# Performance work log

Hardware: AMD Instinct MI355X
Metric: run time of the kernel (lower is better)

Reference implementation:

```python
import jax, jax.numpy as jnp
import numpy as np

# Static dims (match init_kwargs)
N = 20000      # ngene_in == ngene_out
H = 4          # nheads
DIN = 32       # nhidatt_in
D = 32         # nhidatt
E = 640000     # edges per graph
NMETA = 64
SLOPE = 0.2    # DGL GATConv default negative_slope

# hypernetwork_in flat output split sizes (a, w, b, a_out, w_out, b_out)
# a: H*1*(2*DIN)*1=256, w: H*1*DIN=128, b: H*DIN=128, a_out: 1*(2*DIN)=64,
# w_out: (DIN*H)*DIN=4096, b_out: 1*DIN=32  -> total 4704
HIN_OFF = np.cumsum([0, 256, 128, 128, 64, 4096, 32])
# hypernetwork_out1 (L=2 att layers): a: H*3*(2*D)=768, w: H*(DIN+2*D)*D=12288,
# b: H*3*D=384, a_out: 3*(2*D)=192, w_out: (3*D*H)*D=12288, b_out: 3*D=96 -> 26016
HOUT_OFF = np.cumsum([0, 768, 12288, 384, 192, 12288, 96])


def gatconv(src, dst, x, fc_w, bias, attn_l, attn_r, heads, dout):
    """DGL-style GATConv on an edge list (src -> dst), sum-aggregation at dst."""
    feat = (x @ fc_w.T).reshape(N, heads, dout)          # [N,H,D]
    el = jnp.sum(feat * attn_l, axis=-1)                 # [N,H]
    er = jnp.sum(feat * attn_r, axis=-1)                 # [N,H]
    e = jax.nn.leaky_relu(el[src] + er[dst], SLOPE)      # [E,H]
    m = jax.ops.segment_max(e, dst, num_segments=N)      # edge-softmax (stable)
    m = jnp.where(jnp.isfinite(m), m, 0.0)
    ex = jnp.exp(e - m[dst])
    s = jax.ops.segment_sum(ex, dst, num_segments=N)
    alpha = ex / (s[dst] + 1e-9)                         # [E,H]
    out = jax.ops.segment_sum(alpha[:, :, None] * feat[src], dst, num_segments=N)
    return out + bias.reshape(1, heads, dout)            # [N,H,D]


def _split(h, offs):
    return [h[offs[i]:offs[i + 1]] for i in range(len(offs) - 1)]


def setup_inputs() -> dict:
    key = jax.random.key(0)
    ks = jax.random.split(key, 12)
    return {
        "X_in1": jax.random.normal(ks[0], (N,), jnp.float32),
        "metadata_in1": jax.random.normal(ks[1], (NMETA,), jnp.float32),
        "metadata_trg": jax.random.normal(ks[2], (NMETA,), jnp.float32),
        "W_hin": jax.random.normal(ks[3], (NMETA, 4704), jnp.float32) * 0.05,
        "b_hin": jax.random.normal(ks[4], (4704,), jnp.float32) * 0.05,
        "W_hout": jax.random.normal(ks[5], (NMETA, 26016), jnp.float32) * 0.05,
        "b_hout": jax.random.normal(ks[6], (26016,), jnp.float32) * 0.05,
        "src_in": jax.random.randint(ks[7], (E,), 0, N, jnp.int32),
        "dst_in": jax.random.randint(ks[8], (E,), 0, N, jnp.int32),
        "src_trg": jax.random.randint(ks[9], (E,), 0, N, jnp.int32),
        "dst_trg": jax.random.randint(ks[10], (E,), 0, N, jnp.int32),
    }


def reference(X_in1, metadata_in1, metadata_trg, W_hin, b_hin, W_hout, b_hout,
              src_in, dst_in, src_trg, dst_trg):
    # ---- hypernetwork_in(metadata_in1): generate input-GAT params ----
    h = metadata_in1 @ W_hin + b_hin
    a_f, w_f, b_f, ao_f, wo_f, bo_f = _split(h, HIN_OFF)
    a_in = a_f.reshape(H, 1, 2 * DIN, 1)
    w_in = w_f.reshape(H, 1, DIN)
    b_in = b_f.reshape(H, DIN)
    a_out_in = ao_f.reshape(1, 2 * DIN)
    w_out_in = wo_f.reshape(DIN * H, DIN)
    b_out_in = bo_f.reshape(1, DIN)

    # ---- gat() helper on g_in1 (attentions1 + out_att1) ----
    a_tmp = a_in[:, 0, :, :].reshape(2, H, -1)           # exact torch reshape
    w_tmp = w_in[:, :1, :].reshape(-1, 1)                # [H*DIN, 1]
    b_tmp = b_in[:, :DIN].reshape(-1)                    # [H*DIN]
    ao_tmp = a_out_in[0, :].reshape(2, -1)
    wo_tmp = w_out_in[:DIN * H, :].reshape(-1, DIN * H)  # [DIN, DIN*H]
    bo_tmp = b_out_in[0, :]

    x = X_in1[:N].reshape(-1, 1)
    z = gatconv(src_in, dst_in, x, w_tmp, b_tmp,
                a_tmp[0].reshape(1, H, -1), a_tmp[1].reshape(1, H, -1),
                H, DIN).reshape(N, -1)                   # [N, H*DIN]
    z_1 = jax.nn.elu(gatconv(src_in, dst_in, z, wo_tmp, bo_tmp,
                             ao_tmp[0].reshape(1, 1, -1), ao_tmp[1].reshape(1, 1, -1),
                             1, DIN)).reshape(N, -1)     # [N, DIN]

    # ---- hypernetwork_out1(metadata_trg): params for attentions3/4 ----
    h2 = metadata_trg @ W_hout + b_hout
    a_f, w_f, b_f, ao_f, wo_f, bo_f = _split(h2, HOUT_OFF)
    a = a_f.reshape(H, -1, 2 * D, 1)                     # [H, 3, 2D, 1]
    w = w_f.reshape(H, -1, D)                            # [H, DIN+2D, D]
    b = b_f.reshape(H, -1)                               # [H, 3D]
    a_out = ao_f.reshape(-1, 2 * D)                      # [3, 2D]
    w_out = wo_f.reshape(-1, D)                          # [3*D*H, D]
    b_out = bo_f.reshape(-1, D)                          # [3, D]

    # ---- attentions3 / out_att3 on g_trg_in ----
    a_t = a[:, 0, :, :].reshape(2, H, -1)
    w_t = w[:, :DIN, :].reshape(-1, DIN)                 # [H*D, DIN]
    b_t = b[:, :D].reshape(-1)
    ao_t = a_out[0, :].reshape(2, -1)
    wo_t = w_out[:D * H, :].reshape(-1, D * H)
    bo_t = b_out[0, :]
    z2 = gatconv(src_trg, dst_trg, z_1, w_t, b_t,
                 a_t[0].reshape(1, H, -1), a_t[1].reshape(1, H, -1),
                 H, D).reshape(N, -1)
    z2 = jax.nn.elu(gatconv(src_trg, dst_trg, z2, wo_t, bo_t,
                            ao_t[0].reshape(1, 1, -1), ao_t[1].reshape(1, 1, -1),
                            1, D)).reshape(N, D)

    # ---- attentions4 / out_att4 on g_trg_in ----
    a_t2 = a[:, 1, :, :].reshape(2, H, -1)
    w_t2 = w[:, DIN:DIN + D, :].reshape(-1, D)
    b_t2 = b[:, D:2 * D].reshape(-1)
    ao_t2 = a_out[1, :].reshape(2, -1)
    wo_t2 = w_out[D * H:2 * D * H, :].reshape(-1, D * H)
    bo_t2 = b_out[1, :]
    z2 = gatconv(src_trg, dst_trg, z2, w_t2, b_t2,
                 a_t2[0].reshape(1, H, -1), a_t2[1].reshape(1, H, -1),
                 H, D).reshape(N, -1)
    z2 = jax.nn.elu(gatconv(src_trg, dst_trg, z2, wo_t2, bo_t2,
                            ao_t2[0].reshape(1, 1, -1), ao_t2[1].reshape(1, 1, -1),
                            1, D)).reshape(N, D)
    return z2
```

## Files before the change

### kernel.cpp

```cpp
#include <hip/hip_runtime.h>
#include <math.h>

#define NN 20000
#define EE 640000
#define NB4C 5000
#define NCH 80
#define CHE 8000

typedef unsigned short ushortT;
typedef unsigned int uintT;

__device__ __forceinline__ float lrelu(float x){ return x >= 0.f ? x : 0.2f*x; }
__device__ __forceinline__ ushortT f2bf(float x){
  uintT u = __float_as_uint(x);
  u = (u + 0x7FFFu + ((u >> 16) & 1u)) >> 16;
  return (ushortT)u;
}
__device__ __forceinline__ float bfl(uintT w){ return __uint_as_float(w << 16); }
__device__ __forceinline__ float bfh(uintT w){ return __uint_as_float(w & 0xFFFF0000u); }

__global__ __launch_bounds__(256) void k_prmhist(const float* __restrict__ m1,
        const float* __restrict__ mt, const float* __restrict__ Whin,
        const float* __restrict__ bhin, const float* __restrict__ Whout,
        const float* __restrict__ bhout, float* __restrict__ P,
        const int* __restrict__ dst_in, const int* __restrict__ dst_trg,
        int* __restrict__ histB){
  __shared__ int hist[NN/2];
  int b = blockIdx.x;
  if (b < 2*NCH){
    int g = b / NCH, c = b % NCH;
    const int* dst = g ? dst_trg : dst_in;
    for (int i=threadIdx.x; i<NN/2; i+=256) hist[i] = 0;
    __syncthreads();
    int e0 = c*CHE;
    for (int k=threadIdx.x; k<CHE; k+=256){
      int d = dst[e0+k];
      atomicAdd(&hist[d>>1], (d&1) ? 65536 : 1);
    }
    __syncthreads();
    int* outp = histB + b*(NN/2);
    for (int i=threadIdx.x; i<NN/2; i+=256) outp[i] = hist[i];
    return;
  }
  int t = (b - 2*NCH)*256 + threadIdx.x;
  if (t >= 22048) return;
  int sj; bool inA;
  if      (t < 128)  { sj = 256+t;          inA=true; }
  else if (t < 256)  { sj = 384+(t-128);    inA=true; }
  else if (t < 384)  { sj = t-256;          inA=true; }
  else if (t < 512)  { sj = 128+(t-384);    inA=true; }
  else if (t < 4608) { sj = 576+(t-512);    inA=true; }
  else if (t < 4640) { sj = 4672+(t-4608);  inA=true; }
  else if (t < 4672) { sj = 512+(t-4640);   inA=true; }
  else if (t < 4704) { sj = 544+(t-4672);   inA=true; }
  else { inA=false;
    if      (t < 8800)  { int k=t-4704, o=k>>5, i=k&31; sj = 768 + (o>>5)*3072+(o&31)*32+i; }
    else if (t < 8928)  { int o=t-8800; sj = 13056 + (o>>5)*96+(o&31); }
    else if (t < 9056)  { int q=t-8928;       sj = (q>>6)*192+(q&63); }
    else if (t < 9184)  { int q=(t-9056)+128; sj = (q>>6)*192+(q&63); }
    else if (t < 13280) { sj = 13632 + (t-9184); }
    else if (t < 13312) { sj = 25920 + (t-13280); }
    else if (t < 13344) { sj = 13440 + (t-13312); }
    else if (t < 13376) { sj = 13472 + (t-13344); }
    else if (t < 17472) { int k=t-13376, o=k>>5, i=k&31; sj = 768 + (o>>5)*3072+(32+(o&31))*32+i; }
    else if (t < 17600) { int o=t-17472; sj = 13056 + (o>>5)*96+32+(o&31); }
    else if (t < 17728) { int q=t-17600;       sj = (q>>6)*192+64+(q&63); }
    else if (t < 17856) { int q=(t-17728)+128; sj = (q>>6)*192+64+(q&63); }
    else if (t < 21952) { sj = 13632+4096+(t-17856); }
    else if (t < 21984) { sj = 25920+32+(t-21952); }
    else if (t < 22016) { sj = 13440+64+(t-21984); }
    else                { sj = 13440+96+(t-22016); }
  }
  float acc;
  if (inA){
    acc = bhin[sj];
    #pragma unroll 8
    for (int k=0;k<64;++k) acc = fmaf(m1[k], Whin[k*4704 + sj], acc);
  } else {
    acc = bhout[sj];
    #pragma unroll 8
    for (int k=0;k<64;++k) acc = fmaf(mt[k], Whout[k*26016 + sj], acc);
  }
  P[t] = acc;
}

__global__ __launch_bounds__(1024) void k_csrA(const int* __restrict__ histB,
        int* __restrict__ exc, int* __restrict__ bsum){
  int b = blockIdx.x, t = threadIdx.x;
  int g = b/20, c2 = b%20;
  int i = c2*1024 + t;
  int tot = 0;
  if (i < NN){
    int sh = (i&1)*16;
    for (int cb=0; cb<NCH; ++cb){
      int w = histB[(g*NCH+cb)*(NN/2) + (i>>1)];
      tot += (w >> sh) & 0xFFFF;
    }
  }
  __shared__ int s[1024];
  s[t] = tot;
  __syncthreads();
  for (int d=1; d<1024; d<<=1){
    int v = (t>=d) ? s[t-d] : 0;
    __syncthreads();
    s[t] += v;
    __syncthreads();
  }
  exc[b*1024 + t] = s[t] - tot;
  if (t == 1023) bsum[b] = s[t];
}

__global__ void k_csrB(const int* __restrict__ bsum, int* __restrict__ bbase,
        int* __restrict__ off_in, int* __restrict__ off_trg,
        const float* __restrict__ P, float* __restrict__ P2){
  int t = threadIdx.x;
  if (t < 8){
    int hh = t >> 1, sel = t & 1;
    const float* W = P;
    const float* A = P + 256 + sel*128;
    float c = 0.f;
    #pragma unroll 8
    for (int d=0; d<32; ++d) c = fmaf(W[hh*32+d], A[hh*32+d], c);
    P2[sel*4 + hh] = c;
  } else if (t == 8){
    int base = 0;
    for (int b=0; b<20; ++b){ bbase[b] = base; base += bsum[b]; }
  } else if (t == 9){
    int base = 0;
    for (int b=20; b<40; ++b){ bbase[b] = base; base += bsum[b]; }
  } else if (t == 10) off_in[NN]  = EE;
  else if   (t == 11) off_trg[NN] = EE;
}

__global__ __launch_bounds__(1024) void k_csrC(const int* __restrict__ histB,
        const int* __restrict__ exc, const int* __restrict__ bbase,
        int* __restrict__ off_in, int* __restrict__ off_trg,
        int* __restrict__ bases){
  int b = blockIdx.x, t = threadIdx.x;
  int g = b/20, c2 = b%20;
  int i = c2*1024 + t;
  if (i >= NN) return;
  int* off = g ? off_trg : off_in;
  int running = exc[b*1024 + t] + bbase[b];
  off[i] = running;
  int sh = (i&1)*16;
  for (int cb=0; cb<NCH; ++cb){
    bases[(g*NCH+cb)*NN + i] = running;
    int w = histB[(g*NCH+cb)*(NN/2) + (i>>1)];
    running += (w >> sh) & 0xFFFF;
  }
}

__global__ __launch_bounds__(256) void k_fillL(const int* __restrict__ src_in,
        const int* __restrict__ dst_in, const int* __restrict__ src_trg,
        const int* __restrict__ dst_trg, const int* __restrict__ bases,
        ushortT* __restrict__ csr_in, ushortT* __restrict__ csr_trg){
  int b = blockIdx.x;
  int g = b / (2*NCH);
  int rem = b % (2*NCH);
  int half = rem / NCH, c = rem % NCH;
  const int* src = g ? src_trg : src_in;
  const int* dst = g ? dst_trg : dst_in;
  ushortT* csr = g ? csr_trg : csr_in;
  __shared__ int alloc[NN/2];
  const int* basep = bases + (g*NCH+c)*NN + half*(NN/2);
  for (int i=threadIdx.x; i<NN/2; i+=256) alloc[i] = basep[i];
  __syncthreads();
  int e0 = c*CHE;
  int lo = half*(NN/2);
  for (int k=threadIdx.x; k<CHE; k+=256){
    int d = dst[e0+k];
    int dl = d - lo;
    if ((unsigned)dl < (unsigned)(NN/2)){
      int p = atomicAdd(&alloc[dl], 1);
      csr[p] = (ushortT)src[e0+k];
    }
  }
}

template<int IN, int OUT, int H>
__global__ __launch_bounds__(256) void k_featel(const float* __restrict__ z,
        const float* __restrict__ W, const float* __restrict__ AL,
        const float* __restrict__ AR, ushortT* __restrict__ featb,
        float* __restrict__ el, float* __restrict__ er){
  __shared__ float Ws[IN*(OUT+1)];
  __shared__ float ALs[OUT], ARs[OUT];
  for (int idx=threadIdx.x; idx<IN*OUT; idx+=256){
    int o = idx / IN, i = idx % IN;
    Ws[i*(OUT+1) + o] = W[idx];
  }
  for (int idx=threadIdx.x; idx<OUT; idx+=256){ ALs[idx]=AL[idx]; ARs[idx]=AR[idx]; }
  __syncthreads();
  const int NCHK = (NN*OUT)/256;
  for (int chunk = blockIdx.x; chunk < NCHK; chunk += gridDim.x){
    int tid = chunk*256 + threadIdx.x;
    int n = tid / OUT, o = tid % OUT;
    const float4* z4 = (const float4*)(z + n*IN);
    float acc = 0.f;
    #pragma unroll
    for (int i=0;i<IN/4;++i){
      float4 zv = z4[i];
      acc = fmaf(zv.x, Ws[(4*i+0)*(OUT+1)+o], acc);
      acc = fmaf(zv.y, Ws[(4*i+1)*(OUT+1)+o], acc);
      acc = fmaf(zv.z, Ws[(4*i+2)*(OUT+1)+o], acc);
      acc = fmaf(zv.w, Ws[(4*i+3)*(OUT+1)+o], acc);
    }
    int h = o >> 5, d = o & 31;
    featb[(h*NN + n)*32 + d] = f2bf(acc);
    float a = acc * ALs[o], b = acc * ARs[o];
    #pragma unroll
    for (int msk=1; msk<32; msk<<=1){
      a += __shfl_xor(a, msk);
      b += __shfl_xor(b, msk);
    }
    if (d == 0){
      el[h*NN + n] = a;
      er[h*NN + n] = b;
    }
  }
}

__global__ __launch_bounds__(256) void k_l1(const int* __restrict__ off,
        const ushortT* __restrict__ csr, const float* __restrict__ X,
        const float* __restrict__ P, const float* __restrict__ P2,
        float* __restrict__ out){
  int wv = threadIdx.x >> 6, l = threadIdx.x & 63;
  int n = blockIdx.x*4 + wv;
  if (n >= NN) return;
  int start = off[n], deg = off[n+1] - start;
  int hl = l & 3, jl = l >> 2;
  float cl = P2[hl], cr = P2[4 + hl];
  float xd = X[n];
  float m = -INFINITY, ssum = 0.f, t = 0.f;
  for (int j = jl; j < deg; j += 16){
    int s = csr[start + j];
    float xs = X[s];
    float e = lrelu(xs*cl + xd*cr);
    if (e > m){
      float w = __expf(m - e);
      ssum = ssum*w + 1.f;
      t    = t*w + xs;
      m = e;
    } else {
      float w = __expf(e - m);
      ssum += w;
      t    = fmaf(w, xs, t);
    }
  }
  #pragma unroll
  for (int msk=4; msk<64; msk<<=1){
    float mo = __shfl_xor(m, msk), so = __shfl_xor(ssum, msk), to = __shfl_xor(t, msk);
    float mn = fmaxf(m, mo);
    if (mn > -INFINITY){
      float w1 = __expf(m - mn), w2 = __expf(mo - mn);
      ssum = ssum*w1 + so*w2;
      t    = t*w1 + to*w2;
    }
    m = mn;
  }
  float tv = t / (ssum + 1e-9f);
  float th = __shfl(tv, l >> 4);
  const float2 w2v = *(const float2*)(P + 2*l);
  const float2 b2v = *(const float2*)(P + 128 + 2*l);
  float2 o;
  o.x = fmaf(th, w2v.x, b2v.x);
  o.y = fmaf(th, w2v.y, b2v.y);
  *(float2*)(out + n*128 + 2*l) = o;
}

template<int H, bool ELU>
__global__ __launch_bounds__(256) void k_aggH(const int* __restrict__ off,
        const ushortT* __restrict__ csr, const ushortT* __restrict__ featb,
        const float* __restrict__ el, const float* __restrict__ er,
        const float* __restrict__ bias, float* __restrict__ out){
  __shared__ float2 as_[4][64];
  int wv = threadIdx.x >> 6, l = threadIdx.x & 63;
  int bid = blockIdx.x;
  int h = bid / NB4C, b = bid % NB4C;
  int n = b*4 + wv;
  if (n >= NN) return;
  const float* elh = el + h*NN;
  const ushortT* fh = featb + (size_t)h*NN*32;
  int start = off[n], deg = off[n+1] - start;
  float erl = er[h*NN + n];
  int g = l >> 3, dl = l & 7;
  float4 acc = make_float4(0.f, 0.f, 0.f, 0.f);
  float asum = 0.f;
  if (deg <= 64){
    int s = 0; float e = -INFINITY;
    if (l < deg){ s = csr[start + l]; e = lrelu(elh[s] + erl); }
    float m = e;
    #pragma unroll
    for (int msk=1; msk<64; msk<<=1) m = fmaxf(m, __shfl_xor(m, msk));
    float a = (l < deg) ? __expf(e - m) : 0.f;
    as_[wv][l] = make_float2(a, __int_as_float(s));
    #pragma unroll 4
    for (int jj = 0; jj < deg; jj += 8){
      float2 pr = as_[wv][jj + g];
      float aj = pr.x; int sj = __float_as_int(pr.y);
      uint2 w = *(const uint2*)(fh + sj*32 + 4*dl);
      acc.x = fmaf(aj, bfl(w.x), acc.x);
      acc.y = fmaf(aj, bfh(w.x), acc.y);
      acc.z = fmaf(aj, bfl(w.y), acc.z);
      acc.w = fmaf(aj, bfh(w.y), acc.w);
      asum += aj;
    }
  } else {
    float m = -INFINITY;
    for (int j0 = 0; j0 < deg; j0 += 64){
      int j = j0 + l;
      int s = 0; float e = -INFINITY;
      if (j < deg){ s = csr[start + j]; e = lrelu(elh[s] + erl); }
      float cm = e;
      #pragma unroll
      for (int msk=1; msk<64; msk<<=1) cm = fmaxf(cm, __shfl_xor(cm, msk));
      float mn = fmaxf(m, cm);
      float rs = __expf(m - mn);
      float a = (j < deg) ? __expf(e - mn) : 0.f;
      acc.x *= rs; acc.y *= rs; acc.z *= rs; acc.w *= rs;
      asum *= rs;
      m = mn;
      as_[wv][l] = make_float2(a, __int_as_float(s));
      int cnt = deg - j0; if (cnt > 64) cnt = 64;
      #pragma unroll 4
      for (int jj = 0; jj < cnt; jj += 8){
        float2 pr = as_[wv][jj + g];
        float aj = pr.x; int sj = __float_as_int(pr.y);
        uint2 w = *(const uint2*)(fh + sj*32 + 4*dl);
        acc.x = fmaf(aj, bfl(w.x), acc.x);
        acc.y = fmaf(aj, bfh(w.x), acc.y);
        acc.z = fmaf(aj, bfl(w.y), acc.z);
        acc.w = fmaf(aj, bfh(w.y), acc.w);
        asum += aj;
      }
    }
  }
  #pragma unroll
  for (int msk=8; msk<64; msk<<=1){
    acc.x += __shfl_xor(acc.x, msk);
    acc.y += __shfl_xor(acc.y, msk);
    acc.z += __shfl_xor(acc.z, msk);
    acc.w += __shfl_xor(acc.w, msk);
    asum  += __shfl_xor(asum,  msk);
  }
  float sinv = 1.f/(asum + 1e-9f);
  if (l < 8){
    const float4 b4 = *(const float4*)(bias + h*32 + 4*l);
    float o0 = fmaf(acc.x, sinv, b4.x);
    float o1 = fmaf(acc.y, sinv, b4.y);
    float o2 = fmaf(acc.z, sinv, b4.z);
    float o3 = fmaf(acc.w, sinv, b4.w);
    if (ELU){
      o0 = o0 > 0.f ? o0 : expm1f(o0);
      o1 = o1 > 0.f ? o1 : expm1f(o1);
      o2 = o2 > 0.f ? o2 : expm1f(o2);
      o3 = o3 > 0.f ? o3 : expm1f(o3);
    }
    *(float4*)(out + n*(H*32) + h*32 + 4*l) = make_float4(o0, o1, o2, o3);
  }
}

#define WS_P     0
#define WS_P2    22144
#define WS_EL    22272
#define WS_ER    102272
#define WS_FEAT  262144
#define WS_ZA    2822144
#define WS_ZB    5382144
#define WS_OFFI  6022144
#define WS_OFFT  6042240
#define WS_CSRI  6423552
#define WS_CSRT  6743552
#define WS_TOTAL 7063552
#define WS_HB    (WS_FEAT + 0)
#define WS_BS    (WS_FEAT + 1600000)
#define WS_EXC   (WS_FEAT + 4800000)
#define WS_BSUM  (WS_FEAT + 4841472)
#define WS_BBASE (WS_FEAT + 4841600)

extern "C" void kernel_launch(void* const* d_in, const int* in_sizes, int n_in,
                              void* d_out, int out_size, void* d_ws, size_t ws_size,
                              hipStream_t stream) {
  if (ws_size < (size_t)WS_TOTAL * sizeof(float)) {
    hipMemsetAsync(d_out, 0, (size_t)out_size * sizeof(float), stream);
    return;
  }
  const float* X      = (const float*)d_in[0];
  const float* m1     = (const float*)d_in[1];
  const float* mt     = (const float*)d_in[2];
  const float* Whin   = (const float*)d_in[3];
  const float* bhin   = (const float*)d_in[4];
  const float* Whout  = (const float*)d_in[5];
  const float* bhout  = (const float*)d_in[6];
  const int* src_in   = (const int*)d_in[7];
  const int* dst_in   = (const int*)d_in[8];
  const int* src_trg  = (const int*)d_in[9];
  const int* dst_trg  = (const int*)d_in[10];
  float* out = (float*)d_out;
  float* ws  = (float*)d_ws;

  float* P    = ws + WS_P;
  float* P2   = ws + WS_P2;
  float* el   = ws + WS_EL;
  float* er   = ws + WS_ER;
  ushortT* featb = (ushortT*)(ws + WS_FEAT);
  float* zA   = ws + WS_ZA;
  float* zB   = ws + WS_ZB;
  int* off_in  = (int*)(ws + WS_OFFI);
  int* off_trg = (int*)(ws + WS_OFFT);
  int* histB   = (int*)(ws + WS_HB);
  int* bases   = (int*)(ws + WS_BS);
  int* exc     = (int*)(ws + WS_EXC);
  int* bsum    = (int*)(ws + WS_BSUM);
  int* bbase   = (int*)(ws + WS_BBASE);
  ushortT* csr_in  = (ushortT*)(ws + WS_CSRI);
  ushortT* csr_trg = (ushortT*)(ws + WS_CSRT);

  k_prmhist<<<2*NCH + 87, 256, 0, stream>>>(m1, mt, Whin, bhin, Whout, bhout, P,
                                            dst_in, dst_trg, histB);
  k_csrA<<<40, 1024, 0, stream>>>(histB, exc, bsum);
  k_csrB<<<1, 64, 0, stream>>>(bsum, bbase, off_in, off_trg, P, P2);
  k_csrC<<<40, 1024, 0, stream>>>(histB, exc, bbase, off_in, off_trg, bases);
  k_fillL<<<4*NCH, 256, 0, stream>>>(src_in, dst_in, src_trg, dst_trg, bases,
                                     csr_in, csr_trg);

  k_l1<<<NB4C, 256, 0, stream>>>(off_in, csr_in, X, P, P2, zA);

  k_featel<128,32,1><<<1024, 256, 0, stream>>>(zA, P+512, P+4640, P+4672, featb, el, er);
  k_aggH<1,true><<<NB4C, 256, 0, stream>>>(off_in, csr_in, featb, el, er, P+4608, zB);

  k_featel<32,128,4><<<1024, 256, 0, stream>>>(zB, P+4704, P+8928, P+9056, featb, el, er);
  k_aggH<4,false><<<4*NB4C, 256, 0, stream>>>(off_trg, csr_trg, featb, el, er, P+8800, zA);

  k_featel<128,32,1><<<1024, 256, 0, stream>>>(zA, P+9184, P+13312, P+13344, featb, el, er);
  k_aggH<1,true><<<NB4C, 256, 0, stream>>>(off_trg, csr_trg, featb, el, er, P+13280, zB);

  k_featel<32,128,4><<<1024, 256, 0, stream>>>(zB, P+13376, P+17600, P+17728, featb, el, er);
  k_aggH<4,false><<<4*NB4C, 256, 0, stream>>>(off_trg, csr_trg, featb, el, er, P+17472, zA);

  k_featel<128,32,1><<<1024, 256, 0, stream>>>(zA, P+17856, P+21984, P+22016, featb, el, er);
  k_aggH<1,true><<<NB4C, 256, 0, stream>>>(off_trg, csr_trg, featb, el, er, P+21952, out);
}
```

Before: 253.4 us.

## Fuse feature projections into preceding layer and single-head aggregation kernels

Folds the first 128->32 projection, plus its attention logits, into the layer-1 kernel. It also adds a single-head aggregation kernel that applies the following 32->128 projection in-register and writes the bf16 features and el/er directly. Double-buffered feature and el/er workspaces let consecutive stages read and write different buffers. This removes three separate projection launches and their intermediate z round-trips through global memory. In exchange, the aggregation kernels do more per-node work, use more shared memory, and read weights uncached from global memory.

```diff
diff --git a/kernel.cpp b/kernel.cpp
--- a/kernel.cpp
+++ b/kernel.cpp
@@ -220,10 +220,11 @@
   }
 }
 
-__global__ __launch_bounds__(256) void k_l1(const int* __restrict__ off,
+__global__ __launch_bounds__(256) void k_l1F(const int* __restrict__ off,
         const ushortT* __restrict__ csr, const float* __restrict__ X,
         const float* __restrict__ P, const float* __restrict__ P2,
-        float* __restrict__ out){
+        ushortT* __restrict__ featb, float* __restrict__ el, float* __restrict__ er){
+  __shared__ float zs[4][128];
   int wv = threadIdx.x >> 6, l = threadIdx.x & 63;
   int n = blockIdx.x*4 + wv;
   if (n >= NN) return;
@@ -262,10 +263,142 @@
   float th = __shfl(tv, l >> 4);
   const float2 w2v = *(const float2*)(P + 2*l);
   const float2 b2v = *(const float2*)(P + 128 + 2*l);
-  float2 o;
-  o.x = fmaf(th, w2v.x, b2v.x);
-  o.y = fmaf(th, w2v.y, b2v.y);
-  *(float2*)(out + n*128 + 2*l) = o;
+  zs[wv][2*l]   = fmaf(th, w2v.x, b2v.x);
+  zs[wv][2*l+1] = fmaf(th, w2v.y, b2v.y);
+  int oo = l >> 1, half = l & 1;
+  const float* Wp = P + 512 + oo*128 + half*64;
+  const float* zp = zs[wv] + half*64;
+  float acc = 0.f;
+  #pragma unroll 8
+  for (int i=0;i<64;++i) acc = fmaf(zp[i], Wp[i], acc);
+  acc += __shfl_xor(acc, 1);
+  if (!half) featb[n*32 + oo] = f2bf(acc);
+  float pa = half ? 0.f : acc * P[4640 + oo];
+  float pb = half ? 0.f : acc * P[4672 + oo];
+  #pragma unroll
+  for (int msk=1; msk<64; msk<<=1){ pa += __shfl_xor(pa, msk); pb += __shfl_xor(pb, msk); }
+  if (l == 0){ el[n] = pa; er[n] = pb; }
+}
+
+template<bool ELU, bool FUSE>
+__global__ __launch_bounds__(256) void k_agg1(const int* __restrict__ off,
+        const ushortT* __restrict__ csr, const ushortT* __restrict__ featb,
+        const float* __restrict__ el, const float* __restrict__ er,
+        const float* __restrict__ bias, float* __restrict__ out,
+        const float* __restrict__ Wf, const float* __restrict__ ALf,
+        const float* __restrict__ ARf, ushortT* __restrict__ featb2,
+        float* __restrict__ el2, float* __restrict__ er2){
+  __shared__ float2 as_[4][64];
+  __shared__ float zr[4][32];
+  int wv = threadIdx.x >> 6, l = threadIdx.x & 63;
+  int n = blockIdx.x*4 + wv;
+  if (n >= NN) return;
+  int start = off[n], deg = off[n+1] - start;
+  float erl = er[n];
+  int g = l >> 3, dl = l & 7;
+  float4 acc = make_float4(0.f, 0.f, 0.f, 0.f);
+  float asum = 0.f;
+  if (deg <= 64){
+    int s = 0; float e = -INFINITY;
+    if (l < deg){ s = csr[start + l]; e = lrelu(el[s] + erl); }
+    float m = e;
+    #pragma unroll
+    for (int msk=1; msk<64; msk<<=1) m = fmaxf(m, __shfl_xor(m, msk));
+    float a = (l < deg) ? __expf(e - m) : 0.f;
+    as_[wv][l] = make_float2(a, __int_as_float(s));
+    #pragma unroll 4
+    for (int jj = 0; jj < deg; jj += 8){
+      float2 pr = as_[wv][jj + g];
+      float aj = pr.x; int sj = __float_as_int(pr.y);
+      uint2 w = *(const uint2*)(featb + sj*32 + 4*dl);
+      acc.x = fmaf(aj, bfl(w.x), acc.x);
+      acc.y = fmaf(aj, bfh(w.x), acc.y);
+      acc.z = fmaf(aj, bfl(w.y), acc.z);
+      acc.w = fmaf(aj, bfh(w.y), acc.w);
+      asum += aj;
+    }
+  } else {
+    float m = -INFINITY;
+    for (int j0 = 0; j0 < deg; j0 += 64){
+      int j = j0 + l;
+      int s = 0; float e = -INFINITY;
+      if (j < deg){ s = csr[start + j]; e = lrelu(el[s] + erl); }
+      float cm = e;
+      #pragma unroll
+      for (int msk=1; msk<64; msk<<=1) cm = fmaxf(cm, __shfl_xor(cm, msk));
+      float mn = fmaxf(m, cm);
+      float rs = __expf(m - mn);
+      float a = (j < deg) ? __expf(e - mn) : 0.f;
+      acc.x *= rs; acc.y *= rs; acc.z *= rs; acc.w *= rs;
+      asum *= rs;
+      m = mn;
+      as_[wv][l] = make_float2(a, __int_as_float(s));
+      int cnt = deg - j0; if (cnt > 64) cnt = 64;
+      #pragma unroll 4
+      for (int jj = 0; jj < cnt; jj += 8){
+        float2 pr = as_[wv][jj + g];
+        float aj = pr.x; int sj = __float_as_int(pr.y);
+        uint2 w = *(const uint2*)(featb + sj*32 + 4*dl);
+        acc.x = fmaf(aj, bfl(w.x), acc.x);
+        acc.y = fmaf(aj, bfh(w.x), acc.y);
+        acc.z = fmaf(aj, bfl(w.y), acc.z);
+        acc.w = fmaf(aj, bfh(w.y), acc.w);
+        asum += aj;
+      }
+    }
+  }
+  #pragma unroll
+  for (int msk=8; msk<64; msk<<=1){
+    acc.x += __shfl_xor(acc.x, msk);
+    acc.y += __shfl_xor(acc.y, msk);
+    acc.z += __shfl_xor(acc.z, msk);
+    acc.w += __shfl_xor(acc.w, msk);
+    asum  += __shfl_xor(asum,  msk);
+  }
+  float sinv = 1.f/(asum + 1e-9f);
+  if (l < 8){
+    const float4 b4 = *(const float4*)(bias + 4*l);
+    float o0 = fmaf(acc.x, sinv, b4.x);
+    float o1 = fmaf(acc.y, sinv, b4.y);
+    float o2 = fmaf(acc.z, sinv, b4.z);
+    float o3 = fmaf(acc.w, sinv, b4.w);
+    if (ELU){
+      o0 = o0 > 0.f ? o0 : expm1f(o0);
+      o1 = o1 > 0.f ? o1 : expm1f(o1);
+      o2 = o2 > 0.f ? o2 : expm1f(o2);
+      o3 = o3 > 0.f ? o3 : expm1f(o3);
+    }
+    if (FUSE){
+      zr[wv][4*l+0] = o0; zr[wv][4*l+1] = o1;
+      zr[wv][4*l+2] = o2; zr[wv][4*l+3] = o3;
+    } else {
+      *(float4*)(out + n*32 + 4*l) = make_float4(o0, o1, o2, o3);
+    }
+  }
+  if (FUSE){
+    int o0 = l, o1 = 64 + l;
+    float f0 = 0.f, f1 = 0.f;
+    #pragma unroll 8
+    for (int i=0;i<32;++i){
+      float zi = zr[wv][i];
+      f0 = fmaf(zi, Wf[o0*32+i], f0);
+      f1 = fmaf(zi, Wf[o1*32+i], f1);
+    }
+    int h0 = l >> 5, h1 = 2 + (l >> 5), d = l & 31;
+    featb2[(h0*NN + n)*32 + d] = f2bf(f0);
+    featb2[(h1*NN + n)*32 + d] = f2bf(f1);
+    float pa0 = f0*ALf[o0], pb0 = f0*ARf[o0];
+    float pa1 = f1*ALf[o1], pb1 = f1*ARf[o1];
+    #pragma unroll
+    for (int msk=1; msk<32; msk<<=1){
+      pa0 += __shfl_xor(pa0, msk); pb0 += __shfl_xor(pb0, msk);
+      pa1 += __shfl_xor(pa1, msk); pb1 += __shfl_xor(pb1, msk);
+    }
+    if (d == 0){
+      el2[h0*NN + n] = pa0; er2[h0*NN + n] = pb0;
+      el2[h1*NN + n] = pa1; er2[h1*NN + n] = pb1;
+    }
+  }
 }
 
 template<int H, bool ELU>
@@ -362,11 +495,14 @@
 
 #define WS_P     0
 #define WS_P2    22144
-#define WS_EL    22272
-#define WS_ER    102272
+#define WS_ELA   22272
+#define WS_ELB   102272
 #define WS_FEAT  262144
+#define WS_FEATB 1542144
 #define WS_ZA    2822144
 #define WS_ZB    5382144
+#define WS_ERA   5382144
+#define WS_ERB   5462144
 #define WS_OFFI  6022144
 #define WS_OFFT  6042240
 #define WS_CSRI  6423552
@@ -401,11 +537,13 @@
 
   float* P    = ws + WS_P;
   float* P2   = ws + WS_P2;
-  float* el   = ws + WS_EL;
-  float* er   = ws + WS_ER;
-  ushortT* featb = (ushortT*)(ws + WS_FEAT);
+  float* elA  = ws + WS_ELA;
+  float* elB  = ws + WS_ELB;
+  float* erA  = ws + WS_ERA;
+  float* erB  = ws + WS_ERB;
+  ushortT* fA = (ushortT*)(ws + WS_FEAT);
+  ushortT* fB = (ushortT*)(ws + WS_FEATB);
   float* zA   = ws + WS_ZA;
-  float* zB   = ws + WS_ZB;
   int* off_in  = (int*)(ws + WS_OFFI);
   int* off_trg = (int*)(ws + WS_OFFT);
   int* histB   = (int*)(ws + WS_HB);
@@ -424,20 +562,24 @@
   k_fillL<<<4*NCH, 256, 0, stream>>>(src_in, dst_in, src_trg, dst_trg, bases,
                                      csr_in, csr_trg);
 
-  k_l1<<<NB4C, 256, 0, stream>>>(off_in, csr_in, X, P, P2, zA);
-
-  k_featel<128,32,1><<<1024, 256, 0, stream>>>(zA, P+512, P+4640, P+4672, featb, el, er);
-  k_aggH<1,true><<<NB4C, 256, 0, stream>>>(off_in, csr_in, featb, el, er, P+4608, zB);
-
-  k_featel<32,128,4><<<1024, 256, 0, stream>>>(zB, P+4704, P+8928, P+9056, featb, el, er);
-  k_aggH<4,false><<<4*NB4C, 256, 0, stream>>>(off_trg, csr_trg, featb, el, er, P+8800, zA);
-
-  k_featel<128,32,1><<<1024, 256, 0, stream>>>(zA, P+9184, P+13312, P+13344, featb, el, er);
-  k_aggH<1,true><<<NB4C, 256, 0, stream>>>(off_trg, csr_trg, featb, el, er, P+13280, zB);
-
-  k_featel<32,128,4><<<1024, 256, 0, stream>>>(zB, P+13376, P+17600, P+17728, featb, el, er);
-  k_aggH<4,false><<<4*NB4C, 256, 0, stream>>>(off_trg, csr_trg, featb, el, er, P+17472, zA);
-
-  k_featel<128,32,1><<<1024, 256, 0, stream>>>(zA, P+17856, P+21984, P+22016, featb, el, er);
-  k_aggH<1,true><<<NB4C, 256, 0, stream>>>(off_trg, csr_trg, featb, el, er, P+21952, out);
-}
+  k_l1F<<<NB4C, 256, 0, stream>>>(off_in, csr_in, X, P, P2, fA, elA, erA);
+
+  k_agg1<true,true><<<NB4C, 256, 0, stream>>>(off_in, csr_in, fA, elA, erA,
+        P+4608, nullptr, P+4704, P+8928, P+9056, fB, elB, erB);
+
+  k_aggH<4,false><<<4*NB4C, 256, 0, stream>>>(off_trg, csr_trg, fB, elB, erB,
+        P+8800, zA);
+
+  k_featel<128,32,1><<<1024, 256, 0, stream>>>(zA, P+9184, P+13312, P+13344,
+        fA, elA, erA);
+  k_agg1<true,true><<<NB4C, 256, 0, stream>>>(off_trg, csr_trg, fA, elA, erA,
+        P+13280, nullptr, P+13376, P+17600, P+17728, fB, elB, erB);
+
+  k_aggH<4,false><<<4*NB4C, 256, 0, stream>>>(off_trg, csr_trg, fB, elB, erB,
+        P+17472, zA);
+
+  k_featel<128,32,1><<<1024, 256, 0, stream>>>(zA, P+17856, P+21984, P+22016,
+        fA, elA, erA);
+  k_agg1<true,false><<<NB4C, 256, 0, stream>>>(off_trg, csr_trg, fA, elA, erA,
+        P+21952, out, nullptr, nullptr, nullptr, nullptr, nullptr, nullptr);
+}
```

Result: slower. 311.5 us (+22.9%).
